# Kernel optimization log

Measured on AMD Instinct MI355X. Metric: run time of the kernel, lower is better.

Reference implementation:

```python
import jax, jax.numpy as jnp
import numpy as np

K = 16          # filter order (number of Laplacian powers)
MLP_OUT = 16    # mlp_hid == mlp_out for mlp_nlayers == 1
D_PE = 64       # phi output dim
BN_EPS = 1e-5
B, N, M = 8, 1024, 128
E = 131072


def setup_inputs() -> dict:
    key = jax.random.key(0)
    ks = jax.random.split(key, 12)
    # Symmetric, spectrally-bounded Laplacian surrogate so 15 matrix powers stay finite.
    A = jax.random.normal(ks[0], (B, N, N), dtype=jnp.float32)
    Lap = (A + jnp.swapaxes(A, -1, -2)) * (0.5 / jnp.sqrt(jnp.float32(N)))
    W = jax.random.normal(ks[1], (B, N, M), dtype=jnp.float32)
    edge_index = jax.random.randint(ks[2], (2, E), 0, B * N, dtype=jnp.int64)
    batch = jnp.repeat(jnp.arange(B, dtype=jnp.int64), N)
    # MLP layer (k -> MLP_OUT) + BatchNorm affine params
    lin_w = jax.random.normal(ks[3], (K, MLP_OUT), dtype=jnp.float32) / jnp.sqrt(jnp.float32(K))
    lin_b = jnp.zeros((MLP_OUT,), dtype=jnp.float32)
    bn_gamma = jnp.ones((MLP_OUT,), dtype=jnp.float32)
    bn_beta = jnp.zeros((MLP_OUT,), dtype=jnp.float32)
    # phi: GIN-style 2-layer MLP after neighbor aggregation
    phi_w1 = jax.random.normal(ks[4], (MLP_OUT, D_PE), dtype=jnp.float32) / jnp.sqrt(jnp.float32(MLP_OUT))
    phi_b1 = jnp.zeros((D_PE,), dtype=jnp.float32)
    phi_w2 = jax.random.normal(ks[5], (D_PE, D_PE), dtype=jnp.float32) / jnp.sqrt(jnp.float32(D_PE))
    phi_b2 = jnp.zeros((D_PE,), dtype=jnp.float32)
    return {"Lap": Lap, "W": W, "lin_w": lin_w, "lin_b": lin_b,
            "bn_gamma": bn_gamma, "bn_beta": bn_beta,
            "phi_w1": phi_w1, "phi_b1": phi_b1, "phi_w2": phi_w2, "phi_b2": phi_b2,
            "edge_index": edge_index, "batch": batch}


def _filter(S, W0):
    """Sequential power filter: returns [k, N, M] = [W0, S@W0, S^2@W0, ...]."""
    def step(out, _):
        nxt = S @ out
        return nxt, nxt
    _, rest = jax.lax.scan(step, W0, None, length=K - 1)
    return jnp.concatenate([W0[None], rest], axis=0)


def reference(Lap, W, lin_w, lin_b, bn_gamma, bn_beta,
              phi_w1, phi_b1, phi_w2, phi_b2, edge_index, batch):
    # Batched filter over all graphs: [B, k, N, M] -> [B, N, M, k]
    feat = jax.vmap(_filter)(Lap, W)
    feat = jnp.transpose(feat, (0, 2, 3, 1))
    # Linear over k -> MLP_OUT channels: [B, N, M, C]
    h = feat @ lin_w + lin_b
    # BatchNorm1d (training mode), per-graph statistics over (N, M) per channel,
    # matching the torch per-graph loop where BN sees [M, C, N].
    mean = jnp.mean(h, axis=(1, 2), keepdims=True)
    var = jnp.var(h, axis=(1, 2), keepdims=True)
    h = (h - mean) * jax.lax.rsqrt(var + BN_EPS) * bn_gamma + bn_beta
    h = jax.nn.relu(h)
    # phi: pool random-sample dim M, flatten graphs -> [N_sum, C]
    x = jnp.mean(h, axis=2).reshape(-1, h.shape[-1])
    src, dst = edge_index[0], edge_index[1]
    agg = jax.ops.segment_sum(x[src], dst, num_segments=x.shape[0])
    g = x + agg  # GIN aggregation
    out = jax.nn.relu(g @ phi_w1 + phi_b1) @ phi_w2 + phi_b2  # [N_sum, D_PE]
    return out
```

## Files before the change

kernel.cpp:

```cpp
#include <hip/hip_runtime.h>

#define B 8
#define N 1024
#define M 128
#define KF 16
#define C 16
#define DPE 64
#define NE 131072
#define NV (B*N)
#define NM (N*M)
#define BN_EPS 1e-5f

typedef short bf16x8 __attribute__((ext_vector_type(8)));
typedef float f32x4 __attribute__((ext_vector_type(4)));

__device__ inline unsigned short f2bf_rne(float f) {
    unsigned u = __float_as_uint(f);
    u += 0x7fffu + ((u >> 16) & 1u);
    return (unsigned short)(u >> 16);
}
__device__ inline float bf2f(unsigned short s) {
    return __uint_as_float((unsigned)s << 16);
}
__device__ inline void split_bf16(float v, unsigned short& hi, unsigned short& lo) {
    hi = f2bf_rne(v);
    float hf = __uint_as_float((unsigned)hi << 16);
    lo = f2bf_rne(v - hf);
}
union U4 { uint4 v; unsigned short s[8]; };
union U2 { uint2 v; unsigned short s[4]; };

__device__ __host__ inline size_t SF4(int b, int nsub, int ks, int hl, int l) {
    return ((((size_t)b * 64 + nsub) * 32 + ks) * 2 + hl) * 64 + l;
}
__device__ __host__ inline size_t PF4(int b, int msub, int ks, int hl, int l) {
    return ((((size_t)b * 8 + msub) * 32 + ks) * 2 + hl) * 64 + l;
}
#define PFBUF ((size_t)B * 8 * 32 * 2 * 64)

__global__ __launch_bounds__(256) void prep_all(const float* __restrict__ Lap,
                                                const float* __restrict__ W,
                                                const int* __restrict__ ei,
                                                uint4* __restrict__ Sf,
                                                uint4* __restrict__ Pf,
                                                unsigned short* __restrict__ feat,
                                                int* __restrict__ cnt) {
    __shared__ float T[32][33];
    int blk = blockIdx.x;
    int t = threadIdx.x;
    if (blk < 512) {
        int b = blk & 7, nb = blk >> 3;
        int nl = t >> 4, kg = t & 15;
        int n = nb * 16 + nl;
        const float* row = Lap + ((size_t)b * N + n) * N;
        #pragma unroll
        for (int jj = 0; jj < 8; jj++) {
            int koct = kg + 16 * jj;
            int k0 = koct * 8;
            float4 f0 = *(const float4*)(row + k0);
            float4 f1 = *(const float4*)(row + k0 + 4);
            float e[8] = {f0.x, f0.y, f0.z, f0.w, f1.x, f1.y, f1.z, f1.w};
            U4 hi, lo;
            #pragma unroll
            for (int j = 0; j < 8; j++) split_bf16(e[j], hi.s[j], lo.s[j]);
            int ks = k0 >> 5;
            int lf = nl + 16 * (koct & 3);
            Sf[SF4(b, nb, ks, 0, lf)] = hi.v;
            Sf[SF4(b, nb, ks, 1, lf)] = lo.v;
        }
    } else if (blk < 1536) {
        int r = blk - 512;
        int b = r & 7;
        int tile = r >> 3;
        int nt = tile & 31, mt = tile >> 5;
        int n0 = nt * 32, m0 = mt * 32;
        {
            int nl = t >> 3, mq = t & 7;
            float4 v = *(const float4*)(W + ((size_t)b * N + n0 + nl) * M + m0 + mq * 4);
            T[nl][mq * 4 + 0] = v.x; T[nl][mq * 4 + 1] = v.y;
            T[nl][mq * 4 + 2] = v.z; T[nl][mq * 4 + 3] = v.w;
        }
        __syncthreads();
        {
            int ml = t >> 3, nq = t & 7;
            U2 o;
            o.s[0] = f2bf_rne(T[nq * 4 + 0][ml]);
            o.s[1] = f2bf_rne(T[nq * 4 + 1][ml]);
            o.s[2] = f2bf_rne(T[nq * 4 + 2][ml]);
            o.s[3] = f2bf_rne(T[nq * 4 + 3][ml]);
            unsigned short* plane = feat + (size_t)b * KF * NM;
            *(uint2*)(plane + (size_t)(m0 + ml) * N + n0 + nq * 4) = o.v;
        }
    } else if (blk < 2048) {
        int r0 = blk - 1536;
        int b = r0 & 7;
        int r = (r0 >> 3) * 256 + t;
        int msub = r >> 11, ks = (r >> 6) & 31, l = r & 63;
        int m = 16 * msub + (l & 15);
        U4 hi, lo;
        #pragma unroll
        for (int j = 0; j < 8; j++) {
            int n = 32 * ks + 8 * (l >> 4) + j;
            float v = W[((size_t)b * N + n) * M + m];
            split_bf16(v, hi.s[j], lo.s[j]);
        }
        Pf[PF4(b, msub, ks, 0, l)] = hi.v;
        Pf[PF4(b, msub, ks, 1, l)] = lo.v;
    } else {
        int e = (blk - 2048) * 256 + t;
        bool is64 = (ei[1] == 0 && ei[3] == 0 && ei[5] == 0 && ei[7] == 0);
        int dst = is64 ? ei[2 * (NE + e)] : ei[NE + e];
        atomicAdd(&cnt[dst], 1);
    }
}

__global__ __launch_bounds__(512) void gemm_chain(const uint4* __restrict__ Sf,
                                                  uint4* __restrict__ PfA,
                                                  uint4* __restrict__ PfB,
                                                  unsigned short* __restrict__ feat,
                                                  unsigned* bar) {
    extern __shared__ __align__(16) char smem[];
    uint4* ldsS = (uint4*)smem;
    float* Dl = (float*)(smem + 131072);

    int b = blockIdx.x & 7, bx = blockIdx.x >> 3;
    int t = threadIdx.x;
    int w = t >> 6, lane = t & 63;
    int g = w >> 2, wq = w & 3;
    size_t sbase = SF4(b, 2 * bx, 0, 0, 0);
    int n0 = 32 * bx;

    #pragma unroll
    for (int i = 0; i < 16; i++) ldsS[t + 512 * i] = Sf[sbase + t + 512 * i];
    __syncthreads();

    #pragma unroll 1
    for (int k = 0; k < KF - 1; k++) {
        const uint4* PfIn = (k & 1) ? PfB : PfA;
        uint4* PfOut      = (k & 1) ? PfA : PfB;
        const uint4* Pw0 = PfIn + (size_t)(b * 8 + 2 * wq) * 4096 + (size_t)(16 * g) * 128;
        const uint4* Pw1 = Pw0 + 4096;

        f32x4 acc[2][2] = {};
        uint4 ph[2][2], pl[2][2];
        #pragma unroll
        for (int q = 0; q < 2; q++) {
            ph[q][0] = Pw0[(size_t)q * 128 + lane];
            pl[q][0] = Pw0[(size_t)q * 128 + 64 + lane];
            ph[q][1] = Pw1[(size_t)q * 128 + lane];
            pl[q][1] = Pw1[(size_t)q * 128 + 64 + lane];
        }
        #pragma unroll 2
        for (int ks = 0; ks < 16; ks++) {
            int kg = 16 * g + ks;
            uint4 a0h = ph[ks & 1][0], a0l = pl[ks & 1][0];
            uint4 a1h = ph[ks & 1][1], a1l = pl[ks & 1][1];
            if (ks < 14) {
                ph[ks & 1][0] = Pw0[(size_t)(ks + 2) * 128 + lane];
                pl[ks & 1][0] = Pw0[(size_t)(ks + 2) * 128 + 64 + lane];
                ph[ks & 1][1] = Pw1[(size_t)(ks + 2) * 128 + lane];
                pl[ks & 1][1] = Pw1[(size_t)(ks + 2) * 128 + 64 + lane];
            }
            bf16x8 b0h = __builtin_bit_cast(bf16x8, ldsS[kg * 128 + lane]);
            bf16x8 b0l = __builtin_bit_cast(bf16x8, ldsS[kg * 128 + 64 + lane]);
            bf16x8 b1h = __builtin_bit_cast(bf16x8, ldsS[4096 + kg * 128 + lane]);
            bf16x8 b1l = __builtin_bit_cast(bf16x8, ldsS[4096 + kg * 128 + 64 + lane]);
            bf16x8 A0h = __builtin_bit_cast(bf16x8, a0h);
            bf16x8 A0l = __builtin_bit_cast(bf16x8, a0l);
            bf16x8 A1h = __builtin_bit_cast(bf16x8, a1h);
            bf16x8 A1l = __builtin_bit_cast(bf16x8, a1l);
            acc[0][0] = __builtin_amdgcn_mfma_f32_16x16x32_bf16(A0h, b0h, acc[0][0], 0, 0, 0);
            acc[0][0] = __builtin_amdgcn_mfma_f32_16x16x32_bf16(A0h, b0l, acc[0][0], 0, 0, 0);
            acc[0][0] = __builtin_amdgcn_mfma_f32_16x16x32_bf16(A0l, b0h, acc[0][0], 0, 0, 0);
            acc[0][1] = __builtin_amdgcn_mfma_f32_16x16x32_bf16(A0h, b1h, acc[0][1], 0, 0, 0);
            acc[0][1] = __builtin_amdgcn_mfma_f32_16x16x32_bf16(A0h, b1l, acc[0][1], 0, 0, 0);
            acc[0][1] = __builtin_amdgcn_mfma_f32_16x16x32_bf16(A0l, b1h, acc[0][1], 0, 0, 0);
            acc[1][0] = __builtin_amdgcn_mfma_f32_16x16x32_bf16(A1h, b0h, acc[1][0], 0, 0, 0);
            acc[1][0] = __builtin_amdgcn_mfma_f32_16x16x32_bf16(A1h, b0l, acc[1][0], 0, 0, 0);
            acc[1][0] = __builtin_amdgcn_mfma_f32_16x16x32_bf16(A1l, b0h, acc[1][0], 0, 0, 0);
            acc[1][1] = __builtin_amdgcn_mfma_f32_16x16x32_bf16(A1h, b1h, acc[1][1], 0, 0, 0);
            acc[1][1] = __builtin_amdgcn_mfma_f32_16x16x32_bf16(A1h, b1l, acc[1][1], 0, 0, 0);
            acc[1][1] = __builtin_amdgcn_mfma_f32_16x16x32_bf16(A1l, b1h, acc[1][1], 0, 0, 0);
        }

        if (g == 1) {
            #pragma unroll
            for (int mi = 0; mi < 2; mi++)
                #pragma unroll
                for (int ni = 0; ni < 2; ni++)
                    #pragma unroll
                    for (int r = 0; r < 4; r++) {
                        int m = 32 * wq + 16 * mi + 4 * (lane >> 4) + r;
                        int c = 16 * ni + (lane & 15);
                        Dl[m * 36 + c] = acc[mi][ni][r];
                    }
        }
        __syncthreads();
        if (g == 0) {
            #pragma unroll
            for (int mi = 0; mi < 2; mi++)
                #pragma unroll
                for (int ni = 0; ni < 2; ni++)
                    #pragma unroll
                    for (int r = 0; r < 4; r++) {
                        int m = 32 * wq + 16 * mi + 4 * (lane >> 4) + r;
                        int c = 16 * ni + (lane & 15);
                        Dl[m * 36 + c] += acc[mi][ni][r];
                    }
        }
        __syncthreads();
        {
            int m = t >> 2, c0 = (t & 3) * 8;
            U4 o;
            #pragma unroll
            for (int j = 0; j < 8; j++) o.s[j] = f2bf_rne(Dl[m * 36 + c0 + j]);
            unsigned short* plane = feat + ((size_t)b * KF + (k + 1)) * NM + (size_t)m * N + n0 + c0;
            *(uint4*)plane = o.v;
        }
        if (k < KF - 2) {
            {
                int l = t & 63;
                int m = 16 * w + (l & 15);
                int ncol = 8 * (l >> 4);
                float4 v0 = *(const float4*)&Dl[m * 36 + ncol];
                float4 v1 = *(const float4*)&Dl[m * 36 + ncol + 4];
                float e[8] = {v0.x, v0.y, v0.z, v0.w, v1.x, v1.y, v1.z, v1.w};
                U4 hi, lo;
                #pragma unroll
                for (int j = 0; j < 8; j++) split_bf16(e[j], hi.s[j], lo.s[j]);
                PfOut[PF4(b, w, bx, 0, l)] = hi.v;
                PfOut[PF4(b, w, bx, 1, l)] = lo.v;
            }
            __syncthreads();
            if (t == 0) {
                __hip_atomic_fetch_add(&bar[b * 32], 1u, __ATOMIC_RELAXED,
                                       __HIP_MEMORY_SCOPE_AGENT);
                unsigned target = 32u * (unsigned)(k + 1);
                while (__hip_atomic_load(&bar[b * 32], __ATOMIC_RELAXED,
                                         __HIP_MEMORY_SCOPE_AGENT) < target)
                    __builtin_amdgcn_s_sleep(1);
            }
            __syncthreads();
            asm volatile("buffer_inv sc0\n\ts_waitcnt vmcnt(0)" ::: "memory");
        } else {
            __syncthreads();
        }
    }
}

__global__ __launch_bounds__(256) void bn_stats(const unsigned short* __restrict__ feat,
                                                const float* __restrict__ lin_w,
                                                const float* __restrict__ lin_b,
                                                float* __restrict__ stats) {
    __shared__ float wls[KF * C];
    __shared__ float red[4][2][C];
    int t = threadIdx.x;
    wls[t] = lin_w[t];
    __syncthreads();
    int b = blockIdx.x & 7;
    int i = (blockIdx.x >> 3) * 256 + t;
    const uint2* fb = (const uint2*)(feat + (size_t)b * KF * NM);

    float4 hacc[C];
    #pragma unroll
    for (int c = 0; c < C; c++) {
        float bb = lin_b[c];
        hacc[c] = make_float4(bb, bb, bb, bb);
    }
    for (int kk = 0; kk < KF; kk++) {
        U2 u; u.v = fb[(size_t)kk * (NM / 4) + i];
        float p0 = bf2f(u.s[0]), p1 = bf2f(u.s[1]), p2 = bf2f(u.s[2]), p3 = bf2f(u.s[3]);
        #pragma unroll
        for (int c = 0; c < C; c++) {
            float wv = wls[kk * C + c];
            hacc[c].x = fmaf(p0, wv, hacc[c].x);
            hacc[c].y = fmaf(p1, wv, hacc[c].y);
            hacc[c].z = fmaf(p2, wv, hacc[c].z);
            hacc[c].w = fmaf(p3, wv, hacc[c].w);
        }
    }
    float s[C], ss[C];
    #pragma unroll
    for (int c = 0; c < C; c++) {
        float4 h = hacc[c];
        s[c] = h.x + h.y + h.z + h.w;
        ss[c] = h.x * h.x + h.y * h.y + h.z * h.z + h.w * h.w;
    }
    #pragma unroll
    for (int off = 32; off > 0; off >>= 1)
        #pragma unroll
        for (int c = 0; c < C; c++) {
            s[c] += __shfl_down(s[c], off);
            ss[c] += __shfl_down(ss[c], off);
        }
    if ((t & 63) == 0) {
        int wv = t >> 6;
        #pragma unroll
        for (int c = 0; c < C; c++) { red[wv][0][c] = s[c]; red[wv][1][c] = ss[c]; }
    }
    __syncthreads();
    if (t < 32) {
        int which = t >> 4, c = t & 15;
        float v = red[0][which][c] + red[1][which][c] + red[2][which][c] + red[3][which][c];
        atomicAdd(&stats[b * 32 + which * 16 + c], v);
    }
}

__global__ __launch_bounds__(256) void bn_x(const unsigned short* __restrict__ feat,
                                            const float* __restrict__ lin_w,
                                            const float* __restrict__ lin_b,
                                            const float* __restrict__ gam,
                                            const float* __restrict__ bet,
                                            const float* __restrict__ stats,
                                            float* __restrict__ x) {
    __shared__ float wls[KF * C];
    __shared__ float red[8][32 * 17];
    int t = threadIdx.x;
    wls[t] = lin_w[t];
    __syncthreads();
    int grp = blockIdx.x;
    int b = grp & 7, n0 = (grp >> 3) * 32;
    int nl = t & 31, mg = t >> 5;
    int n = n0 + nl;

    const float inv_nm = 1.0f / (float)NM;
    float sc[C], sh[C], bb[C];
    #pragma unroll
    for (int c = 0; c < C; c++) {
        float mean = stats[b * 32 + c] * inv_nm;
        float var = stats[b * 32 + 16 + c] * inv_nm - mean * mean;
        sc[c] = gam[c] * rsqrtf(var + BN_EPS);
        sh[c] = bet[c] - mean * sc[c];
        bb[c] = lin_b[c];
    }
    const unsigned short* fb = feat + (size_t)b * KF * NM + n;
    float y[C] = {};
    for (int m = mg * 16; m < mg * 16 + 16; m++) {
        float p[KF];
        #pragma unroll
        for (int kk = 0; kk < KF; kk++) p[kk] = bf2f(fb[(size_t)kk * NM + (size_t)m * N]);
        #pragma unroll
        for (int c = 0; c < C; c++) {
            float h = bb[c];
            #pragma unroll
            for (int kk = 0; kk < KF; kk++) h = fmaf(p[kk], wls[kk * C + c], h);
            y[c] += fmaxf(fmaf(h, sc[c], sh[c]), 0.0f);
        }
    }
    #pragma unroll
    for (int c = 0; c < C; c++) red[mg][nl * 17 + c] = y[c];
    __syncthreads();
    #pragma unroll
    for (int q = 0; q < 2; q++) {
        int slot = t + q * 256;
        int snl = slot >> 4, c = slot & 15;
        float v = 0.0f;
        #pragma unroll
        for (int m8 = 0; m8 < 8; m8++) v += red[m8][snl * 17 + c];
        v *= (1.0f / (float)M);
        x[((size_t)b * N + n0 + snl) * C + c] = v;
    }
}

__global__ __launch_bounds__(256) void edge_scan(const int* __restrict__ cnt,
                                                 int* __restrict__ off, int* __restrict__ cur) {
    __shared__ int ss[256];
    int t = threadIdx.x;
    int base = t * 32;
    int local[32];
    int s = 0;
    #pragma unroll
    for (int i = 0; i < 32; i++) { local[i] = cnt[base + i]; s += local[i]; }
    ss[t] = s;
    __syncthreads();
    #pragma unroll
    for (int d = 1; d < 256; d <<= 1) {
        int v = (t >= d) ? ss[t - d] : 0;
        __syncthreads();
        ss[t] += v;
        __syncthreads();
    }
    int excl = ss[t] - s;
    #pragma unroll
    for (int i = 0; i < 32; i++) { off[base + i] = excl; cur[base + i] = excl; excl += local[i]; }
}

__global__ __launch_bounds__(256) void edge_fill(const int* __restrict__ ei,
                                                 int* __restrict__ cur, int* __restrict__ bucket) {
    int e = blockIdx.x * 256 + threadIdx.x;
    bool is64 = (ei[1] == 0 && ei[3] == 0 && ei[5] == 0 && ei[7] == 0);
    int src, dst;
    if (is64) { src = ei[2 * e]; dst = ei[2 * (NE + e)]; }
    else      { src = ei[e];     dst = ei[NE + e]; }
    int pos = atomicAdd(&cur[dst], 1);
    bucket[pos] = src;
}

__global__ __launch_bounds__(256) void phi_fused(const int* __restrict__ cnt,
                                                 const int* __restrict__ off,
                                                 const int* __restrict__ bucket,
                                                 const float* __restrict__ x,
                                                 const float* __restrict__ w1,
                                                 const float* __restrict__ b1,
                                                 const float* __restrict__ w2,
                                                 const float* __restrict__ b2,
                                                 float* __restrict__ out) {
    __shared__ float w1s[C * DPE];
    __shared__ float w2s[DPE * DPE];
    __shared__ float b2s[DPE];
    __shared__ float gsh[16][17];
    __shared__ float h1sh[16][DPE];
    int t = threadIdx.x;
    #pragma unroll
    for (int q = 0; q < 4; q++) w1s[t + q * 256] = w1[t + q * 256];
    #pragma unroll
    for (int q = 0; q < 16; q++) w2s[t + q * 256] = w2[t + q * 256];
    if (t < DPE) b2s[t] = b2[t];

    {
        int nl = t >> 4, c = t & 15;
        int n = blockIdx.x * 16 + nl;
        int o = off[n], d = cnt[n];
        float v = x[(size_t)n * C + c];
        int j = 0;
        for (; j + 4 <= d; j += 4) {
            int s0 = bucket[o + j], s1 = bucket[o + j + 1];
            int s2 = bucket[o + j + 2], s3 = bucket[o + j + 3];
            v += x[(size_t)s0 * C + c];
            v += x[(size_t)s1 * C + c];
            v += x[(size_t)s2 * C + c];
            v += x[(size_t)s3 * C + c];
        }
        for (; j < d; j++) v += x[(size_t)bucket[o + j] * C + c];
        gsh[nl][c] = v;
    }
    __syncthreads();
    #pragma unroll
    for (int q = 0; q < 4; q++) {
        int item = t + 256 * q;
        int node = item >> 6, j = item & 63;
        float h = b1[j];
        #pragma unroll
        for (int c = 0; c < C; c++) h = fmaf(gsh[node][c], w1s[c * DPE + j], h);
        h1sh[node][j] = fmaxf(h, 0.0f);
    }
    __syncthreads();
    #pragma unroll
    for (int q = 0; q < 4; q++) {
        int item = t + 256 * q;
        int node = item >> 6, d = item & 63;
        float o2 = b2s[d];
        #pragma unroll
        for (int j = 0; j < DPE; j++) o2 = fmaf(h1sh[node][j], w2s[j * DPE + d], o2);
        out[((size_t)blockIdx.x * 16 + node) * DPE + d] = o2;
    }
}

extern "C" void kernel_launch(void* const* d_in, const int* in_sizes, int n_in,
                              void* d_out, int out_size, void* d_ws, size_t ws_size,
                              hipStream_t stream) {
    const float* Lap   = (const float*)d_in[0];
    const float* W     = (const float*)d_in[1];
    const float* lin_w = (const float*)d_in[2];
    const float* lin_b = (const float*)d_in[3];
    const float* gam   = (const float*)d_in[4];
    const float* bet   = (const float*)d_in[5];
    const float* w1    = (const float*)d_in[6];
    const float* b1    = (const float*)d_in[7];
    const float* w2    = (const float*)d_in[8];
    const float* b2    = (const float*)d_in[9];
    const int*   ei    = (const int*)d_in[10];

    char* wsb = (char*)d_ws;
    unsigned short* feat = (unsigned short*)wsb;
    uint4* Sf    = (uint4*)(wsb + ((size_t)32 << 20));
    uint4* Pf    = (uint4*)(wsb + ((size_t)64 << 20));
    float* stats = (float*)(wsb + ((size_t)72 << 20));
    unsigned* bar = (unsigned*)(stats + 256);
    float* x     = stats + 2048;
    int*   cnt   = (int*)(x + (size_t)NV * C);
    int*   off   = cnt + NV;
    int*   cur   = off + NV;
    int*   bucket= cur + NV;
    float* out   = (float*)d_out;

    static bool attr_set = false;
    if (!attr_set) {
        hipFuncSetAttribute((const void*)gemm_chain,
                            hipFuncAttributeMaxDynamicSharedMemorySize, 149504);
        attr_set = true;
    }

    hipMemsetAsync(stats, 0, 8192, stream);
    hipMemsetAsync(cnt, 0, NV * sizeof(int), stream);
    prep_all<<<dim3(2560), 256, 0, stream>>>(Lap, W, ei, Sf, Pf, feat, cnt);
    gemm_chain<<<dim3(256), 512, 149504, stream>>>(Sf, Pf, Pf + PFBUF, feat, bar);
    bn_stats<<<dim3(1024), 256, 0, stream>>>(feat, lin_w, lin_b, stats);
    bn_x<<<dim3(256), 256, 0, stream>>>(feat, lin_w, lin_b, gam, bet, stats, x);
    edge_scan<<<dim3(1), 256, 0, stream>>>(cnt, off, cur);
    edge_fill<<<dim3(NE / 256), 256, 0, stream>>>(ei, cur, bucket);
    phi_fused<<<dim3(NV / 16), 256, 0, stream>>>(cnt, off, bucket, x, w1, b1, w2, b2, out);
}
```

Baseline: 293.1 us.

## Fuse BN stats/apply and edge CSR build with grid barriers, relayout feat

Switches the feat layout to n-major (m contiguous), so the W copy becomes a plain converting copy and the gemm writes transposed rows. bn_stats and bn_x are merged into one kernel that uses a per-graph spin barrier between the statistics pass and the normalise-and-pool pass. Edge counting, the scan and the fill are merged into one kernel with global spin barriers. The goal is fewer launches and better locality in the BN apply pass. The cost is spin-waits that rely on every block being resident at once, and the bn pass now runs on only 256 blocks.

```diff
diff --git a/kernel.cpp b/kernel.cpp
--- a/kernel.cpp
+++ b/kernel.cpp
@@ -40,12 +40,9 @@
 
 __global__ __launch_bounds__(256) void prep_all(const float* __restrict__ Lap,
                                                 const float* __restrict__ W,
-                                                const int* __restrict__ ei,
                                                 uint4* __restrict__ Sf,
                                                 uint4* __restrict__ Pf,
-                                                unsigned short* __restrict__ feat,
-                                                int* __restrict__ cnt) {
-    __shared__ float T[32][33];
+                                                unsigned short* __restrict__ feat) {
     int blk = blockIdx.x;
     int t = threadIdx.x;
     if (blk < 512) {
@@ -71,27 +68,13 @@
     } else if (blk < 1536) {
         int r = blk - 512;
         int b = r & 7;
-        int tile = r >> 3;
-        int nt = tile & 31, mt = tile >> 5;
-        int n0 = nt * 32, m0 = mt * 32;
-        {
-            int nl = t >> 3, mq = t & 7;
-            float4 v = *(const float4*)(W + ((size_t)b * N + n0 + nl) * M + m0 + mq * 4);
-            T[nl][mq * 4 + 0] = v.x; T[nl][mq * 4 + 1] = v.y;
-            T[nl][mq * 4 + 2] = v.z; T[nl][mq * 4 + 3] = v.w;
-        }
-        __syncthreads();
-        {
-            int ml = t >> 3, nq = t & 7;
-            U2 o;
-            o.s[0] = f2bf_rne(T[nq * 4 + 0][ml]);
-            o.s[1] = f2bf_rne(T[nq * 4 + 1][ml]);
-            o.s[2] = f2bf_rne(T[nq * 4 + 2][ml]);
-            o.s[3] = f2bf_rne(T[nq * 4 + 3][ml]);
-            unsigned short* plane = feat + (size_t)b * KF * NM;
-            *(uint2*)(plane + (size_t)(m0 + ml) * N + n0 + nq * 4) = o.v;
-        }
-    } else if (blk < 2048) {
+        int idx = (r >> 3) * 256 + t;
+        float4 v = *(const float4*)(W + (size_t)b * NM + (size_t)idx * 4);
+        U2 o;
+        o.s[0] = f2bf_rne(v.x); o.s[1] = f2bf_rne(v.y);
+        o.s[2] = f2bf_rne(v.z); o.s[3] = f2bf_rne(v.w);
+        *(uint2*)(feat + (size_t)b * KF * NM + (size_t)idx * 4) = o.v;
+    } else {
         int r0 = blk - 1536;
         int b = r0 & 7;
         int r = (r0 >> 3) * 256 + t;
@@ -106,11 +89,6 @@
         }
         Pf[PF4(b, msub, ks, 0, l)] = hi.v;
         Pf[PF4(b, msub, ks, 1, l)] = lo.v;
-    } else {
-        int e = (blk - 2048) * 256 + t;
-        bool is64 = (ei[1] == 0 && ei[3] == 0 && ei[5] == 0 && ei[7] == 0);
-        int dst = is64 ? ei[2 * (NE + e)] : ei[NE + e];
-        atomicAdd(&cnt[dst], 1);
     }
 }
 
@@ -210,11 +188,11 @@
         }
         __syncthreads();
         {
-            int m = t >> 2, c0 = (t & 3) * 8;
+            int n = t & 31, m0 = (t >> 5) * 8;
             U4 o;
             #pragma unroll
-            for (int j = 0; j < 8; j++) o.s[j] = f2bf_rne(Dl[m * 36 + c0 + j]);
-            unsigned short* plane = feat + ((size_t)b * KF + (k + 1)) * NM + (size_t)m * N + n0 + c0;
+            for (int j = 0; j < 8; j++) o.s[j] = f2bf_rne(Dl[(m0 + j) * 36 + n]);
+            unsigned short* plane = feat + ((size_t)b * KF + (k + 1)) * NM + (size_t)(n0 + n) * M + m0;
             *(uint4*)plane = o.v;
         }
         if (k < KF - 2) {
@@ -248,43 +226,51 @@
     }
 }
 
-__global__ __launch_bounds__(256) void bn_stats(const unsigned short* __restrict__ feat,
+__global__ __launch_bounds__(256) void bn_fused(const unsigned short* __restrict__ feat,
                                                 const float* __restrict__ lin_w,
                                                 const float* __restrict__ lin_b,
-                                                float* __restrict__ stats) {
+                                                const float* __restrict__ gam,
+                                                const float* __restrict__ bet,
+                                                float* __restrict__ stats,
+                                                unsigned* __restrict__ bnbar,
+                                                float* __restrict__ x) {
     __shared__ float wls[KF * C];
     __shared__ float red[4][2][C];
+    __shared__ float st[2 * C];
     int t = threadIdx.x;
     wls[t] = lin_w[t];
     __syncthreads();
-    int b = blockIdx.x & 7;
-    int i = (blockIdx.x >> 3) * 256 + t;
+    int b = blockIdx.x & 7, sub = blockIdx.x >> 3;
     const uint2* fb = (const uint2*)(feat + (size_t)b * KF * NM);
 
-    float4 hacc[C];
-    #pragma unroll
-    for (int c = 0; c < C; c++) {
-        float bb = lin_b[c];
-        hacc[c] = make_float4(bb, bb, bb, bb);
-    }
-    for (int kk = 0; kk < KF; kk++) {
-        U2 u; u.v = fb[(size_t)kk * (NM / 4) + i];
-        float p0 = bf2f(u.s[0]), p1 = bf2f(u.s[1]), p2 = bf2f(u.s[2]), p3 = bf2f(u.s[3]);
+    float s[C] = {}, ss[C] = {};
+    #pragma unroll
+    for (int chunk = 0; chunk < 4; chunk++) {
+        int i = sub * 1024 + chunk * 256 + t;
+        float4 hq[C];
         #pragma unroll
         for (int c = 0; c < C; c++) {
-            float wv = wls[kk * C + c];
-            hacc[c].x = fmaf(p0, wv, hacc[c].x);
-            hacc[c].y = fmaf(p1, wv, hacc[c].y);
-            hacc[c].z = fmaf(p2, wv, hacc[c].z);
-            hacc[c].w = fmaf(p3, wv, hacc[c].w);
-        }
-    }
-    float s[C], ss[C];
-    #pragma unroll
-    for (int c = 0; c < C; c++) {
-        float4 h = hacc[c];
-        s[c] = h.x + h.y + h.z + h.w;
-        ss[c] = h.x * h.x + h.y * h.y + h.z * h.z + h.w * h.w;
+            float bb = lin_b[c];
+            hq[c] = make_float4(bb, bb, bb, bb);
+        }
+        for (int kk = 0; kk < KF; kk++) {
+            U2 u; u.v = fb[(size_t)kk * (NM / 4) + i];
+            float p0 = bf2f(u.s[0]), p1 = bf2f(u.s[1]), p2 = bf2f(u.s[2]), p3 = bf2f(u.s[3]);
+            #pragma unroll
+            for (int c = 0; c < C; c++) {
+                float wv = wls[kk * C + c];
+                hq[c].x = fmaf(p0, wv, hq[c].x);
+                hq[c].y = fmaf(p1, wv, hq[c].y);
+                hq[c].z = fmaf(p2, wv, hq[c].z);
+                hq[c].w = fmaf(p3, wv, hq[c].w);
+            }
+        }
+        #pragma unroll
+        for (int c = 0; c < C; c++) {
+            float4 h = hq[c];
+            s[c] += h.x + h.y + h.z + h.w;
+            ss[c] += h.x * h.x + h.y * h.y + h.z * h.z + h.w * h.w;
+        }
     }
     #pragma unroll
     for (int off = 32; off > 0; off >>= 1)
@@ -304,94 +290,130 @@
         float v = red[0][which][c] + red[1][which][c] + red[2][which][c] + red[3][which][c];
         atomicAdd(&stats[b * 32 + which * 16 + c], v);
     }
-}
-
-__global__ __launch_bounds__(256) void bn_x(const unsigned short* __restrict__ feat,
-                                            const float* __restrict__ lin_w,
-                                            const float* __restrict__ lin_b,
-                                            const float* __restrict__ gam,
-                                            const float* __restrict__ bet,
-                                            const float* __restrict__ stats,
-                                            float* __restrict__ x) {
-    __shared__ float wls[KF * C];
-    __shared__ float red[8][32 * 17];
-    int t = threadIdx.x;
-    wls[t] = lin_w[t];
-    __syncthreads();
-    int grp = blockIdx.x;
-    int b = grp & 7, n0 = (grp >> 3) * 32;
-    int nl = t & 31, mg = t >> 5;
-    int n = n0 + nl;
+    __syncthreads();
+    if (t == 0) {
+        __hip_atomic_fetch_add(&bnbar[b * 32], 1u, __ATOMIC_RELAXED, __HIP_MEMORY_SCOPE_AGENT);
+        while (__hip_atomic_load(&bnbar[b * 32], __ATOMIC_RELAXED, __HIP_MEMORY_SCOPE_AGENT) < 32u)
+            __builtin_amdgcn_s_sleep(1);
+    }
+    __syncthreads();
+    if (t < 32) {
+        float* sp = &stats[b * 32 + t];
+        st[t] = __hip_atomic_load(sp, __ATOMIC_RELAXED, __HIP_MEMORY_SCOPE_AGENT);
+    }
+    __syncthreads();
 
     const float inv_nm = 1.0f / (float)NM;
-    float sc[C], sh[C], bb[C];
+    float sc[C], sh[C], bb2[C];
     #pragma unroll
     for (int c = 0; c < C; c++) {
-        float mean = stats[b * 32 + c] * inv_nm;
-        float var = stats[b * 32 + 16 + c] * inv_nm - mean * mean;
+        float mean = st[c] * inv_nm;
+        float var = st[16 + c] * inv_nm - mean * mean;
         sc[c] = gam[c] * rsqrtf(var + BN_EPS);
         sh[c] = bet[c] - mean * sc[c];
-        bb[c] = lin_b[c];
-    }
-    const unsigned short* fb = feat + (size_t)b * KF * NM + n;
+        bb2[c] = lin_b[c];
+    }
+    int n0 = sub * 32;
+    int nl = t >> 3, mlane = t & 7;
+    int n = n0 + nl;
+    const unsigned short* fn = feat + (size_t)b * KF * NM + (size_t)n * M;
     float y[C] = {};
-    for (int m = mg * 16; m < mg * 16 + 16; m++) {
-        float p[KF];
-        #pragma unroll
-        for (int kk = 0; kk < KF; kk++) p[kk] = bf2f(fb[(size_t)kk * NM + (size_t)m * N]);
+    #pragma unroll
+    for (int chunk = 0; chunk < 4; chunk++) {
+        int m0 = mlane * 4 + chunk * 32;
+        float4 hq[C];
         #pragma unroll
         for (int c = 0; c < C; c++) {
-            float h = bb[c];
+            float bb = bb2[c];
+            hq[c] = make_float4(bb, bb, bb, bb);
+        }
+        for (int kk = 0; kk < KF; kk++) {
+            U2 u; u.v = *(const uint2*)(fn + (size_t)kk * NM + m0);
+            float p0 = bf2f(u.s[0]), p1 = bf2f(u.s[1]), p2 = bf2f(u.s[2]), p3 = bf2f(u.s[3]);
             #pragma unroll
-            for (int kk = 0; kk < KF; kk++) h = fmaf(p[kk], wls[kk * C + c], h);
-            y[c] += fmaxf(fmaf(h, sc[c], sh[c]), 0.0f);
-        }
-    }
-    #pragma unroll
-    for (int c = 0; c < C; c++) red[mg][nl * 17 + c] = y[c];
-    __syncthreads();
-    #pragma unroll
-    for (int q = 0; q < 2; q++) {
-        int slot = t + q * 256;
-        int snl = slot >> 4, c = slot & 15;
-        float v = 0.0f;
-        #pragma unroll
-        for (int m8 = 0; m8 < 8; m8++) v += red[m8][snl * 17 + c];
-        v *= (1.0f / (float)M);
-        x[((size_t)b * N + n0 + snl) * C + c] = v;
-    }
-}
-
-__global__ __launch_bounds__(256) void edge_scan(const int* __restrict__ cnt,
-                                                 int* __restrict__ off, int* __restrict__ cur) {
-    __shared__ int ss[256];
+            for (int c = 0; c < C; c++) {
+                float wv = wls[kk * C + c];
+                hq[c].x = fmaf(p0, wv, hq[c].x);
+                hq[c].y = fmaf(p1, wv, hq[c].y);
+                hq[c].z = fmaf(p2, wv, hq[c].z);
+                hq[c].w = fmaf(p3, wv, hq[c].w);
+            }
+        }
+        #pragma unroll
+        for (int c = 0; c < C; c++) {
+            float4 h = hq[c];
+            y[c] += fmaxf(fmaf(h.x, sc[c], sh[c]), 0.0f);
+            y[c] += fmaxf(fmaf(h.y, sc[c], sh[c]), 0.0f);
+            y[c] += fmaxf(fmaf(h.z, sc[c], sh[c]), 0.0f);
+            y[c] += fmaxf(fmaf(h.w, sc[c], sh[c]), 0.0f);
+        }
+    }
+    #pragma unroll
+    for (int off = 4; off > 0; off >>= 1)
+        #pragma unroll
+        for (int c = 0; c < C; c++) y[c] += __shfl_down(y[c], off);
+    if (mlane == 0) {
+        #pragma unroll
+        for (int c = 0; c < C; c++)
+            x[((size_t)b * N + n) * C + c] = y[c] * (1.0f / (float)M);
+    }
+}
+
+__global__ __launch_bounds__(256) void edge_build(const int* __restrict__ ei,
+                                                  int* __restrict__ cnt,
+                                                  int* __restrict__ off,
+                                                  int* __restrict__ cur,
+                                                  int* __restrict__ bucket,
+                                                  unsigned* __restrict__ ebar) {
+    __shared__ int sscan[256];
     int t = threadIdx.x;
-    int base = t * 32;
-    int local[32];
-    int s = 0;
-    #pragma unroll
-    for (int i = 0; i < 32; i++) { local[i] = cnt[base + i]; s += local[i]; }
-    ss[t] = s;
-    __syncthreads();
-    #pragma unroll
-    for (int d = 1; d < 256; d <<= 1) {
-        int v = (t >= d) ? ss[t - d] : 0;
-        __syncthreads();
-        ss[t] += v;
-        __syncthreads();
-    }
-    int excl = ss[t] - s;
-    #pragma unroll
-    for (int i = 0; i < 32; i++) { off[base + i] = excl; cur[base + i] = excl; excl += local[i]; }
-}
-
-__global__ __launch_bounds__(256) void edge_fill(const int* __restrict__ ei,
-                                                 int* __restrict__ cur, int* __restrict__ bucket) {
-    int e = blockIdx.x * 256 + threadIdx.x;
+    int e = blockIdx.x * 256 + t;
     bool is64 = (ei[1] == 0 && ei[3] == 0 && ei[5] == 0 && ei[7] == 0);
     int src, dst;
     if (is64) { src = ei[2 * e]; dst = ei[2 * (NE + e)]; }
     else      { src = ei[e];     dst = ei[NE + e]; }
+    atomicAdd(&cnt[dst], 1);
+    __syncthreads();
+    if (t == 0) {
+        __hip_atomic_fetch_add(&ebar[0], 1u, __ATOMIC_RELAXED, __HIP_MEMORY_SCOPE_AGENT);
+        while (__hip_atomic_load(&ebar[0], __ATOMIC_RELAXED, __HIP_MEMORY_SCOPE_AGENT) < 512u)
+            __builtin_amdgcn_s_sleep(1);
+    }
+    __syncthreads();
+    if (blockIdx.x == 0) {
+        int base = t * 32;
+        int local[32];
+        int s = 0;
+        #pragma unroll
+        for (int i = 0; i < 32; i++) {
+            local[i] = __hip_atomic_load(&cnt[base + i], __ATOMIC_RELAXED, __HIP_MEMORY_SCOPE_AGENT);
+            s += local[i];
+        }
+        sscan[t] = s;
+        __syncthreads();
+        #pragma unroll
+        for (int d = 1; d < 256; d <<= 1) {
+            int v = (t >= d) ? sscan[t - d] : 0;
+            __syncthreads();
+            sscan[t] += v;
+            __syncthreads();
+        }
+        int excl = sscan[t] - s;
+        #pragma unroll
+        for (int i = 0; i < 32; i++) {
+            __hip_atomic_store(&off[base + i], excl, __ATOMIC_RELAXED, __HIP_MEMORY_SCOPE_AGENT);
+            __hip_atomic_store(&cur[base + i], excl, __ATOMIC_RELAXED, __HIP_MEMORY_SCOPE_AGENT);
+            excl += local[i];
+        }
+        __syncthreads();
+        if (t == 0)
+            __hip_atomic_store(&ebar[64], 1u, __ATOMIC_RELAXED, __HIP_MEMORY_SCOPE_AGENT);
+    }
+    if (t == 0) {
+        while (__hip_atomic_load(&ebar[64], __ATOMIC_RELAXED, __HIP_MEMORY_SCOPE_AGENT) == 0u)
+            __builtin_amdgcn_s_sleep(1);
+    }
+    __syncthreads();
     int pos = atomicAdd(&cur[dst], 1);
     bucket[pos] = src;
 }
@@ -476,7 +498,9 @@
     uint4* Sf    = (uint4*)(wsb + ((size_t)32 << 20));
     uint4* Pf    = (uint4*)(wsb + ((size_t)64 << 20));
     float* stats = (float*)(wsb + ((size_t)72 << 20));
-    unsigned* bar = (unsigned*)(stats + 256);
+    unsigned* bar   = (unsigned*)((char*)stats + 1024);
+    unsigned* bnbar = (unsigned*)((char*)stats + 2048);
+    unsigned* ebar  = (unsigned*)((char*)stats + 4096);
     float* x     = stats + 2048;
     int*   cnt   = (int*)(x + (size_t)NV * C);
     int*   off   = cnt + NV;
@@ -493,11 +517,9 @@
 
     hipMemsetAsync(stats, 0, 8192, stream);
     hipMemsetAsync(cnt, 0, NV * sizeof(int), stream);
-    prep_all<<<dim3(2560), 256, 0, stream>>>(Lap, W, ei, Sf, Pf, feat, cnt);
+    prep_all<<<dim3(2048), 256, 0, stream>>>(Lap, W, Sf, Pf, feat);
     gemm_chain<<<dim3(256), 512, 149504, stream>>>(Sf, Pf, Pf + PFBUF, feat, bar);
-    bn_stats<<<dim3(1024), 256, 0, stream>>>(feat, lin_w, lin_b, stats);
-    bn_x<<<dim3(256), 256, 0, stream>>>(feat, lin_w, lin_b, gam, bet, stats, x);
-    edge_scan<<<dim3(1), 256, 0, stream>>>(cnt, off, cur);
-    edge_fill<<<dim3(NE / 256), 256, 0, stream>>>(ei, cur, bucket);
+    bn_fused<<<dim3(256), 256, 0, stream>>>(feat, lin_w, lin_b, gam, bet, stats, bnbar, x);
+    edge_build<<<dim3(512), 256, 0, stream>>>(ei, cnt, off, cur, bucket, ebar);
     phi_fused<<<dim3(NV / 16), 256, 0, stream>>>(cnt, off, bucket, x, w1, b1, w2, b2, out);
 }
```

Result: slower. 338.1 us (+15.3%).
